# Optimization experiments

Hardware: AMD Instinct MI355X
Metric: run time of the kernel (lower is better)

## Reference

```python
import jax, jax.numpy as jnp
import numpy as np

TOKENS = 64
IN_F = 8192
OUT_F = 8192
CODESZ = 8
CB_SIZE = 256


def fwht(x):
    """Sylvester fast Walsh-Hadamard transform along last dim. x: (B, n), n power of 2."""
    b, n = x.shape
    h = 1
    while h < n:
        x = x.reshape(b, n // (2 * h), 2, h)
        x = jnp.concatenate([x[:, :, :1] + x[:, :, 1:], x[:, :, :1] - x[:, :, 1:]], axis=2)
        x = x.reshape(b, n)
        h *= 2
    return x


def setup_inputs() -> dict:
    key = jax.random.key(0)
    k0, k1, k2, k3, k4, k5 = jax.random.split(key, 6)
    x = jax.random.normal(k0, (TOKENS, IN_F), jnp.float32)
    # SU/SV are random sign vectors in QuIP
    SU = jnp.sign(jax.random.normal(k1, (IN_F,), jnp.float32))
    SV = jnp.sign(jax.random.normal(k2, (OUT_F,), jnp.float32))
    grid = jax.random.normal(k3, (CB_SIZE, CODESZ), jnp.float32)  # codebook entries
    Wscale = jnp.ones((1,), jnp.float32)
    bias = jax.random.normal(k4, (OUT_F,), jnp.float32) * 0.01
    Qidxs = jax.random.randint(k5, (OUT_F, IN_F // CODESZ), 0, CB_SIZE, jnp.int32)
    return {"x": x, "SU": SU, "SV": SV, "grid": grid, "Wscale": Wscale, "bias": bias, "Qidxs": Qidxs}


def reference(x, SU, SV, grid, Wscale, bias, Qidxs):
    # 1) input sign scale
    xs = x * SU
    # 2) matmul_hadUt with folded wscale: x @ H^T / sqrt(n_in) * wscale (H symmetric Sylvester)
    inv_sqrt_in = 1.0 / jnp.sqrt(jnp.asarray(IN_F, x.dtype))
    xh = fwht(xs) * (inv_sqrt_in * Wscale[0])
    # 3) codebook dequant + matmul: W_hat[o, i] from codebook lookup, out = xh @ W_hat^T
    W_hat = grid[Qidxs].reshape(OUT_F, IN_F)  # (out, in) dequantized weight
    y = xh @ W_hat.T  # (tokens, out)
    # 4) matmul_hadU on the output side, truncate to out_features (no-op here: q_out == out)
    inv_sqrt_out = 1.0 / jnp.sqrt(jnp.asarray(OUT_F, x.dtype))
    yh = fwht(y) * inv_sqrt_out
    yh = yh[..., :OUT_F]
    # 5) output sign scale + bias
    return yh * SV + bias
```

## Files before the change

### kernel.cpp

```cpp
#include <hip/hip_runtime.h>
#include <hip/hip_bf16.h>

#define TOKENS 64
#define IN_F 8192
#define OUT_F 8192
#define CB 256

typedef _Float16 half8 __attribute__((ext_vector_type(8)));
typedef float f32x4 __attribute__((ext_vector_type(4)));

__global__ __launch_bounds__(256) void k_fwht_in(const float* __restrict__ x,
                                                 const float* __restrict__ SU,
                                                 const float* __restrict__ Wscale,
                                                 _Float16* __restrict__ xh_frag)
{
    __shared__ float buf[256 * 33];
    __shared__ _Float16 xrowP[256 * 40];
    const int t    = threadIdx.x;
    const int lane = t & 63;
    const int w    = t >> 6;
    const int row  = blockIdx.x;

    float v[32];
    const float* xr = x + row * IN_F;
#pragma unroll
    for (int rh = 0; rh < 8; ++rh) {
        int base = (rh << 10) | (t << 2);
        float4 xv = *(const float4*)(xr + base);
        float4 sv = *(const float4*)(SU + base);
        v[rh * 4 + 0] = xv.x * sv.x;
        v[rh * 4 + 1] = xv.y * sv.y;
        v[rh * 4 + 2] = xv.z * sv.z;
        v[rh * 4 + 3] = xv.w * sv.w;
    }
#pragma unroll
    for (int h = 1; h < 32; h <<= 1) {
#pragma unroll
        for (int r = 0; r < 32; ++r) {
            if ((r & h) == 0) {
                float a = v[r], b = v[r + h];
                v[r] = a + b;
                v[r + h] = a - b;
            }
        }
    }
#pragma unroll
    for (int m = 1; m < 64; m <<= 1) {
        bool upper = (lane & m) != 0;
#pragma unroll
        for (int r = 0; r < 32; ++r) {
            float p = __shfl_xor(v[r], m, 64);
            v[r] = upper ? (p - v[r]) : (v[r] + p);
        }
    }
#pragma unroll
    for (int r = 0; r < 32; ++r) buf[t * 33 + r] = v[r];
    __syncthreads();
    {
        float s1 = (w & 1) ? -1.f : 1.f;
        float s2 = (w & 2) ? -1.f : 1.f;
        float s3 = s1 * s2;
#pragma unroll
        for (int r = 0; r < 32; ++r) {
            float a0 = buf[(0 * 64 + lane) * 33 + r];
            float a1 = buf[(1 * 64 + lane) * 33 + r];
            float a2 = buf[(2 * 64 + lane) * 33 + r];
            float a3 = buf[(3 * 64 + lane) * 33 + r];
            v[r] = a0 + s1 * a1 + s2 * a2 + s3 * a3;
        }
    }
    const float scale = 0.011048543456039806f * Wscale[0];
#pragma unroll
    for (int r = 0; r < 32; ++r) {
        int c = ((r >> 2) << 10) | (t << 2) | (r & 3);
        int idx = (c & 31) + (c >> 5) * 40;
        xrowP[idx] = (_Float16)(v[r] * scale);
    }
    __syncthreads();
    {
        const int mt  = row >> 4;
        const int l15 = row & 15;
        _Float16* base = xh_frag + ((size_t)(t * 4 + mt) * 64 + l15) * 8;
#pragma unroll
        for (int g = 0; g < 4; ++g) {
            half8 val = *(const half8*)&xrowP[t * 40 + g * 8];
            *(half8*)(base + g * 16 * 8) = val;
        }
    }
}

#define SQ_STRIDE 261
__global__ __launch_bounds__(256, 2) void k_qgemm(const _Float16* __restrict__ xh_frag,
                                                  const int* __restrict__ Qidxs,
                                                  const float* __restrict__ grid,
                                                  float* __restrict__ y_part)
{
    __shared__ __align__(16) _Float16 glds[CB * 8];
    __shared__ __align__(16) char uni[4 * 64 * 68 * 4];
    int*   sq  = (int*)uni;
    float* red = (float*)uni;

    const int tid = threadIdx.x;
    const int g   = blockIdx.x >> 2;
    const int p   = blockIdx.x & 3;
    const int n0  = g * 64;

    {
        const float4* gp = (const float4*)grid + tid * 2;
        float4 g0 = gp[0];
        float4 g1 = gp[1];
        _Float16* gl = &glds[tid * 8];
        gl[0] = (_Float16)g0.x; gl[1] = (_Float16)g0.y;
        gl[2] = (_Float16)g0.z; gl[3] = (_Float16)g0.w;
        gl[4] = (_Float16)g1.x; gl[5] = (_Float16)g1.y;
        gl[6] = (_Float16)g1.z; gl[7] = (_Float16)g1.w;
    }
#pragma unroll
    for (int i = 0; i < 16; ++i) {
        int idx4 = i * 256 + tid;
        int r  = idx4 >> 6;
        int c4 = idx4 & 63;
        int4 vv = *(const int4*)(Qidxs + (size_t)(n0 + r) * 1024 + p * 256 + c4 * 4);
        int* dst = &sq[r * SQ_STRIDE + c4 * 4];
        dst[0] = vv.x; dst[1] = vv.y; dst[2] = vv.z; dst[3] = vv.w;
    }
    __syncthreads();

    const int lane = tid & 63;
    const int w    = tid >> 6;
    const int col  = lane & 15;
    const int quad = lane >> 4;

    const int cbase = w * 64 + quad;
#define QGATHER(dst4, s)                                              \
    {                                                                 \
        int cc = cbase + (s) * 4;                                     \
        dst4.x = sq[(0 * 16 + col) * SQ_STRIDE + cc];                 \
        dst4.y = sq[(1 * 16 + col) * SQ_STRIDE + cc];                 \
        dst4.z = sq[(2 * 16 + col) * SQ_STRIDE + cc];                 \
        dst4.w = sq[(3 * 16 + col) * SQ_STRIDE + cc];                 \
    }

    const _Float16* abase = xh_frag + ((size_t)(p * 64 + w * 16) * 4 * 64 + lane) * 8;

    f32x4 acc[4][4] = {};

    int4 qv1, qv2;
    half8 b_c[4];
    {
        int4 qv0;
        QGATHER(qv0, 0);
        QGATHER(qv1, 1);
        QGATHER(qv2, 2);
        b_c[0] = *(const half8*)&glds[qv0.x * 8];
        b_c[1] = *(const half8*)&glds[qv0.y * 8];
        b_c[2] = *(const half8*)&glds[qv0.z * 8];
        b_c[3] = *(const half8*)&glds[qv0.w * 8];
    }
    half8 a_c[4], a_n[4];
#pragma unroll
    for (int mt = 0; mt < 4; ++mt) {
        a_c[mt] = *(const half8*)(abase + (size_t)(0 * 4 + mt) * 512);
        a_n[mt] = *(const half8*)(abase + (size_t)(1 * 4 + mt) * 512);
    }

#pragma unroll 4
    for (int s = 0; s < 16; ++s) {
        const int s3 = (s + 3 < 16 ? s + 3 : 15);
        const int s2 = (s + 2 < 16 ? s + 2 : 15);
        int4 qn;
        QGATHER(qn, s3);
        half8 b_n[4], a_nn[4];
        b_n[0] = *(const half8*)&glds[qv1.x * 8];
        b_n[1] = *(const half8*)&glds[qv1.y * 8];
        b_n[2] = *(const half8*)&glds[qv1.z * 8];
        b_n[3] = *(const half8*)&glds[qv1.w * 8];
#pragma unroll
        for (int mt = 0; mt < 4; ++mt)
            a_nn[mt] = *(const half8*)(abase + (size_t)(s2 * 4 + mt) * 512);
#pragma unroll
        for (int nt = 0; nt < 4; ++nt)
#pragma unroll
            for (int mt = 0; mt < 4; ++mt)
                acc[nt][mt] = __builtin_amdgcn_mfma_f32_16x16x32_f16(
                    a_c[mt], b_c[nt], acc[nt][mt], 0, 0, 0);
#pragma unroll
        for (int nt = 0; nt < 4; ++nt) b_c[nt] = b_n[nt];
        qv1 = qv2; qv2 = qn;
#pragma unroll
        for (int mt = 0; mt < 4; ++mt) { a_c[mt] = a_n[mt]; a_n[mt] = a_nn[mt]; }
    }

    __syncthreads();
#pragma unroll
    for (int nt = 0; nt < 4; ++nt)
#pragma unroll
        for (int mt = 0; mt < 4; ++mt)
#pragma unroll
            for (int i = 0; i < 4; ++i) {
                int r = mt * 16 + quad * 4 + i;
                int c = nt * 16 + col;
                red[(w * 64 + r) * 68 + c] = acc[nt][mt][i];
            }
    __syncthreads();
    float* yp = y_part + (size_t)p * TOKENS * OUT_F;
#pragma unroll
    for (int j = 0; j < 16; ++j) {
        int idx = j * 256 + tid;
        int rr = idx >> 6, cc = idx & 63;
        float s = (red[(0 * 64 + rr) * 68 + cc] + red[(1 * 64 + rr) * 68 + cc])
                + (red[(2 * 64 + rr) * 68 + cc] + red[(3 * 64 + rr) * 68 + cc]);
        yp[(size_t)rr * OUT_F + n0 + cc] = s;
    }
#undef QGATHER
}

__global__ __launch_bounds__(256) void k_fwht_out(const float* __restrict__ y_part,
                                                  const float* __restrict__ SV,
                                                  const float* __restrict__ bias,
                                                  float* __restrict__ out)
{
    __shared__ float buf[256 * 33];
    const int t    = threadIdx.x;
    const int lane = t & 63;
    const int w    = t >> 6;
    const int row  = blockIdx.x;

    const float* y0 = y_part + (size_t)row * OUT_F;
    const size_t ps = (size_t)TOKENS * OUT_F;

    float v[32];
#pragma unroll
    for (int rh = 0; rh < 8; ++rh) {
        int base = (rh << 10) | (t << 2);
        float4 a = *(const float4*)(y0 + base);
        float4 b = *(const float4*)(y0 + ps + base);
        float4 c = *(const float4*)(y0 + 2 * ps + base);
        float4 d = *(const float4*)(y0 + 3 * ps + base);
        v[rh * 4 + 0] = (a.x + b.x) + (c.x + d.x);
        v[rh * 4 + 1] = (a.y + b.y) + (c.y + d.y);
        v[rh * 4 + 2] = (a.z + b.z) + (c.z + d.z);
        v[rh * 4 + 3] = (a.w + b.w) + (c.w + d.w);
    }
#pragma unroll
    for (int h = 1; h < 32; h <<= 1) {
#pragma unroll
        for (int r = 0; r < 32; ++r) {
            if ((r & h) == 0) {
                float a = v[r], b = v[r + h];
                v[r] = a + b;
                v[r + h] = a - b;
            }
        }
    }
#pragma unroll
    for (int m = 1; m < 64; m <<= 1) {
        bool upper = (lane & m) != 0;
#pragma unroll
        for (int r = 0; r < 32; ++r) {
            float p = __shfl_xor(v[r], m, 64);
            v[r] = upper ? (p - v[r]) : (v[r] + p);
        }
    }
#pragma unroll
    for (int r = 0; r < 32; ++r) buf[t * 33 + r] = v[r];
    __syncthreads();
    {
        float s1 = (w & 1) ? -1.f : 1.f;
        float s2 = (w & 2) ? -1.f : 1.f;
        float s3 = s1 * s2;
#pragma unroll
        for (int r = 0; r < 32; ++r) {
            float a0 = buf[(0 * 64 + lane) * 33 + r];
            float a1 = buf[(1 * 64 + lane) * 33 + r];
            float a2 = buf[(2 * 64 + lane) * 33 + r];
            float a3 = buf[(3 * 64 + lane) * 33 + r];
            v[r] = a0 + s1 * a1 + s2 * a2 + s3 * a3;
        }
    }
    const float scale = 0.011048543456039806f;
    float* oo = out + (size_t)row * OUT_F;
#pragma unroll
    for (int rh = 0; rh < 8; ++rh) {
        int base = (rh << 10) | (t << 2);
        float4 sv = *(const float4*)(SV + base);
        float4 bv = *(const float4*)(bias + base);
        float4 o;
        o.x = v[rh * 4 + 0] * scale * sv.x + bv.x;
        o.y = v[rh * 4 + 1] * scale * sv.y + bv.y;
        o.z = v[rh * 4 + 2] * scale * sv.z + bv.z;
        o.w = v[rh * 4 + 3] * scale * sv.w + bv.w;
        *(float4*)(oo + base) = o;
    }
}

extern "C" void kernel_launch(void* const* d_in, const int* in_sizes, int n_in,
                              void* d_out, int out_size, void* d_ws, size_t ws_size,
                              hipStream_t stream) {
    const float* x      = (const float*)d_in[0];
    const float* SU     = (const float*)d_in[1];
    const float* SV     = (const float*)d_in[2];
    const float* grid   = (const float*)d_in[3];
    const float* Wscale = (const float*)d_in[4];
    const float* bias   = (const float*)d_in[5];
    const int*   Qidxs  = (const int*)d_in[6];
    float* out = (float*)d_out;

    _Float16* xh_frag = (_Float16*)d_ws;
    float*    y_part  = (float*)((char*)d_ws + ((size_t)1 << 20));

    k_fwht_in<<<TOKENS, 256, 0, stream>>>(x, SU, Wscale, xh_frag);
    k_qgemm<<<512, 256, 0, stream>>>(xh_frag, Qidxs, grid, y_part);
    k_fwht_out<<<TOKENS, 256, 0, stream>>>(y_part, SV, bias, out);
}
```

Baseline: 112.6 us.

## Pack codebook indices into bytes in per-wave LDS and shrink reduction buffer

The qgemm kernel now packs four 8-bit codebook indices into one 32-bit word per lane and keeps them in a per-wave shared region laid out so each wave loads and reads only its own slice. That removes the block-wide barrier after staging and cuts LDS reads per step from four gathers to four packed words, with a shift and mask to pick the index. The epilogue reduction reuses the smaller 17-stride buffer one 16-column tile at a time, which shrinks LDS use and may allow more occupancy, at the cost of extra barriers in the epilogue. Masking indices to 8 bits assumes the codebook has 256 entries.

```diff
diff --git a/kernel.cpp b/kernel.cpp
--- a/kernel.cpp
+++ b/kernel.cpp
@@ -89,73 +89,79 @@
     }
 }
 
-#define SQ_STRIDE 261
+#define SQWW 17
 __global__ __launch_bounds__(256, 2) void k_qgemm(const _Float16* __restrict__ xh_frag,
                                                   const int* __restrict__ Qidxs,
                                                   const float* __restrict__ grid,
                                                   float* __restrict__ y_part)
 {
     __shared__ __align__(16) _Float16 glds[CB * 8];
-    __shared__ __align__(16) char uni[4 * 64 * 68 * 4];
-    int*   sq  = (int*)uni;
+    __shared__ __align__(16) unsigned int uni[4 * 64 * SQWW];
     float* red = (float*)uni;
 
-    const int tid = threadIdx.x;
-    const int g   = blockIdx.x >> 2;
-    const int p   = blockIdx.x & 3;
-    const int n0  = g * 64;
-
-    {
-        const float4* gp = (const float4*)grid + tid * 2;
-        float4 g0 = gp[0];
-        float4 g1 = gp[1];
-        _Float16* gl = &glds[tid * 8];
-        gl[0] = (_Float16)g0.x; gl[1] = (_Float16)g0.y;
-        gl[2] = (_Float16)g0.z; gl[3] = (_Float16)g0.w;
-        gl[4] = (_Float16)g1.x; gl[5] = (_Float16)g1.y;
-        gl[6] = (_Float16)g1.z; gl[7] = (_Float16)g1.w;
-    }
-#pragma unroll
-    for (int i = 0; i < 16; ++i) {
-        int idx4 = i * 256 + tid;
-        int r  = idx4 >> 6;
-        int c4 = idx4 & 63;
-        int4 vv = *(const int4*)(Qidxs + (size_t)(n0 + r) * 1024 + p * 256 + c4 * 4);
-        int* dst = &sq[r * SQ_STRIDE + c4 * 4];
-        dst[0] = vv.x; dst[1] = vv.y; dst[2] = vv.z; dst[3] = vv.w;
-    }
-    __syncthreads();
-
+    const int tid  = threadIdx.x;
     const int lane = tid & 63;
     const int w    = tid >> 6;
     const int col  = lane & 15;
     const int quad = lane >> 4;
-
-    const int cbase = w * 64 + quad;
-#define QGATHER(dst4, s)                                              \
-    {                                                                 \
-        int cc = cbase + (s) * 4;                                     \
-        dst4.x = sq[(0 * 16 + col) * SQ_STRIDE + cc];                 \
-        dst4.y = sq[(1 * 16 + col) * SQ_STRIDE + cc];                 \
-        dst4.z = sq[(2 * 16 + col) * SQ_STRIDE + cc];                 \
-        dst4.w = sq[(3 * 16 + col) * SQ_STRIDE + cc];                 \
+    const int g    = blockIdx.x >> 2;
+    const int p    = blockIdx.x & 3;
+    const int n0   = g * 64;
+
+    unsigned int* sqw = uni + w * (64 * SQWW);
+
+    {
+        const int* qbase = Qidxs + (size_t)n0 * 1024 + p * 256 + w * 64 + col * 4;
+#pragma unroll
+        for (int i = 0; i < 16; ++i) {
+            int r = i * 4 + quad;
+            int4 vv = *(const int4*)(qbase + (size_t)r * 1024);
+            unsigned int pk = (unsigned int)(vv.x & 255) |
+                              ((unsigned int)(vv.y & 255) << 8) |
+                              ((unsigned int)(vv.z & 255) << 16) |
+                              ((unsigned int)(vv.w & 255) << 24);
+            sqw[r * SQWW + col] = pk;
+        }
+    }
+    {
+#pragma unroll
+        for (int e = 0; e < 4; ++e) {
+            int entry = lane + 64 * e;
+            float4 g0 = *((const float4*)grid + entry * 2);
+            float4 g1 = *((const float4*)grid + entry * 2 + 1);
+            half8 hv;
+            hv[0] = (_Float16)g0.x; hv[1] = (_Float16)g0.y;
+            hv[2] = (_Float16)g0.z; hv[3] = (_Float16)g0.w;
+            hv[4] = (_Float16)g1.x; hv[5] = (_Float16)g1.y;
+            hv[6] = (_Float16)g1.z; hv[7] = (_Float16)g1.w;
+            *(half8*)&glds[entry * 8] = hv;
+        }
+    }
+    __asm__ volatile("s_waitcnt lgkmcnt(0)" ::: "memory");
+    __builtin_amdgcn_sched_barrier(0);
+
+    const int shq = quad * 8;
+
+#define QWREAD(dst, s_)                                              \
+    {                                                                \
+        dst[0] = sqw[(0 * 16 + col) * SQWW + (s_)];                  \
+        dst[1] = sqw[(1 * 16 + col) * SQWW + (s_)];                  \
+        dst[2] = sqw[(2 * 16 + col) * SQWW + (s_)];                  \
+        dst[3] = sqw[(3 * 16 + col) * SQWW + (s_)];                  \
     }
 
     const _Float16* abase = xh_frag + ((size_t)(p * 64 + w * 16) * 4 * 64 + lane) * 8;
 
     f32x4 acc[4][4] = {};
 
-    int4 qv1, qv2;
+    unsigned int qw_c[4], qw_n[4];
+    QWREAD(qw_c, 0);
+    QWREAD(qw_n, 1);
     half8 b_c[4];
-    {
-        int4 qv0;
-        QGATHER(qv0, 0);
-        QGATHER(qv1, 1);
-        QGATHER(qv2, 2);
-        b_c[0] = *(const half8*)&glds[qv0.x * 8];
-        b_c[1] = *(const half8*)&glds[qv0.y * 8];
-        b_c[2] = *(const half8*)&glds[qv0.z * 8];
-        b_c[3] = *(const half8*)&glds[qv0.w * 8];
+#pragma unroll
+    for (int nt = 0; nt < 4; ++nt) {
+        unsigned int q = (qw_c[nt] >> shq) & 255u;
+        b_c[nt] = *(const half8*)&glds[q * 8];
     }
     half8 a_c[4], a_n[4];
 #pragma unroll
@@ -166,18 +172,18 @@
 
 #pragma unroll 4
     for (int s = 0; s < 16; ++s) {
-        const int s3 = (s + 3 < 16 ? s + 3 : 15);
-        const int s2 = (s + 2 < 16 ? s + 2 : 15);
-        int4 qn;
-        QGATHER(qn, s3);
+        const int s2q = (s + 2 < 16 ? s + 2 : 15);
+        unsigned int qw_nn[4];
+        QWREAD(qw_nn, s2q);
         half8 b_n[4], a_nn[4];
-        b_n[0] = *(const half8*)&glds[qv1.x * 8];
-        b_n[1] = *(const half8*)&glds[qv1.y * 8];
-        b_n[2] = *(const half8*)&glds[qv1.z * 8];
-        b_n[3] = *(const half8*)&glds[qv1.w * 8];
+#pragma unroll
+        for (int nt = 0; nt < 4; ++nt) {
+            unsigned int q = (qw_n[nt] >> shq) & 255u;
+            b_n[nt] = *(const half8*)&glds[q * 8];
+        }
 #pragma unroll
         for (int mt = 0; mt < 4; ++mt)
-            a_nn[mt] = *(const half8*)(abase + (size_t)(s2 * 4 + mt) * 512);
+            a_nn[mt] = *(const half8*)(abase + (size_t)(s2q * 4 + mt) * 512);
 #pragma unroll
         for (int nt = 0; nt < 4; ++nt)
 #pragma unroll
@@ -185,34 +191,35 @@
                 acc[nt][mt] = __builtin_amdgcn_mfma_f32_16x16x32_f16(
                     a_c[mt], b_c[nt], acc[nt][mt], 0, 0, 0);
 #pragma unroll
-        for (int nt = 0; nt < 4; ++nt) b_c[nt] = b_n[nt];
-        qv1 = qv2; qv2 = qn;
+        for (int nt = 0; nt < 4; ++nt) { b_c[nt] = b_n[nt]; qw_n[nt] = qw_nn[nt]; }
 #pragma unroll
         for (int mt = 0; mt < 4; ++mt) { a_c[mt] = a_n[mt]; a_n[mt] = a_nn[mt]; }
     }
 
-    __syncthreads();
-#pragma unroll
-    for (int nt = 0; nt < 4; ++nt)
+    float* redw = red + w * (64 * SQWW);
+    float* yp = y_part + (size_t)p * TOKENS * OUT_F;
+#pragma unroll
+    for (int nt = 0; nt < 4; ++nt) {
 #pragma unroll
         for (int mt = 0; mt < 4; ++mt)
 #pragma unroll
             for (int i = 0; i < 4; ++i) {
                 int r = mt * 16 + quad * 4 + i;
-                int c = nt * 16 + col;
-                red[(w * 64 + r) * 68 + c] = acc[nt][mt][i];
+                redw[r * SQWW + col] = acc[nt][mt][i];
             }
-    __syncthreads();
-    float* yp = y_part + (size_t)p * TOKENS * OUT_F;
-#pragma unroll
-    for (int j = 0; j < 16; ++j) {
-        int idx = j * 256 + tid;
-        int rr = idx >> 6, cc = idx & 63;
-        float s = (red[(0 * 64 + rr) * 68 + cc] + red[(1 * 64 + rr) * 68 + cc])
-                + (red[(2 * 64 + rr) * 68 + cc] + red[(3 * 64 + rr) * 68 + cc]);
-        yp[(size_t)rr * OUT_F + n0 + cc] = s;
-    }
-#undef QGATHER
+        __syncthreads();
+#pragma unroll
+        for (int j = 0; j < 4; ++j) {
+            int idx = j * 256 + tid;
+            int rr = idx >> 4;
+            int cc = idx & 15;
+            float s = (red[(0 * 64 + rr) * SQWW + cc] + red[(1 * 64 + rr) * SQWW + cc])
+                    + (red[(2 * 64 + rr) * SQWW + cc] + red[(3 * 64 + rr) * SQWW + cc]);
+            yp[(size_t)rr * OUT_F + n0 + nt * 16 + cc] = s;
+        }
+        __syncthreads();
+    }
+#undef QWREAD
 }
 
 __global__ __launch_bounds__(256) void k_fwht_out(const float* __restrict__ y_part,
```

After: 110.8 us. Within noise of the previous version (-1.6%).
